# Kernel optimization log

Hardware: AMD Instinct MI355X
Metric: run time of the kernel (lower is better)

## Reference

```python
import jax, jax.numpy as jnp
import numpy as np

T, B, DIM, N = 2048, 16, 1024, 64
INIT_BETA_BIAS = 2.0
EPS = 1e-6


def setup_inputs() -> dict:
    key = jax.random.key(0)
    ks = jax.random.split(key, 6)
    xavier = np.sqrt(2.0 / (N + DIM)).astype(np.float32)
    return {
        "x": jax.random.normal(ks[0], (T, B, DIM), dtype=jnp.float32),
        "S0": jnp.zeros((B, N, N), dtype=jnp.float32),
        "W_k": jax.random.normal(ks[1], (N, DIM), dtype=jnp.float32) * xavier,
        "W_v": jax.random.normal(ks[2], (N, DIM), dtype=jnp.float32) * xavier,
        "W_q": jax.random.normal(ks[3], (N, DIM), dtype=jnp.float32) * xavier,
        "W_beta": jax.random.normal(ks[4], (N, DIM), dtype=jnp.float32) * xavier,
        "b_beta": jnp.full((N,), INIT_BETA_BIAS, dtype=jnp.float32),
    }


def reference(x, S0, W_k, W_v, W_q, W_beta, b_beta):
    # Batched projections: [T, B, dim] @ [dim, n] -> [T, B, n]
    k_all = jnp.einsum("tbd,nd->tbn", x, W_k)
    v_all = jnp.einsum("tbd,nd->tbn", x, W_v)
    q_all = jnp.einsum("tbd,nd->tbn", x, W_q)
    g_all = jax.nn.sigmoid(jnp.einsum("tbd,nd->tbn", x, W_beta) + b_beta)

    def step(S, inp):
        k, v, q, g = inp  # each [B, n]
        k_norm = k / (jnp.linalg.norm(k, axis=-1, keepdims=True) + EPS)
        retrieved = jnp.einsum("bij,bj->bi", S, k_norm)
        delta = v - retrieved
        S_new = g[:, :, None] * S + delta[:, :, None] * k_norm[:, None, :]
        Sq = jnp.einsum("bij,bj->bi", S_new, q)
        out = Sq * jax.nn.silu(Sq)  # self-gated output
        return S_new, out

    S_final, output = jax.lax.scan(step, S0, (k_all, v_all, q_all, g_all))
    return output, S_final
```

## Files before the change

kernel.cpp:

```cpp
#include <hip/hip_runtime.h>
#include <math.h>

#define T_STEPS 2048
#define BATCH   16
#define DIM     1024
#define NSTATE  64
#define NFIELD  256
#define PROJ_TSTRIDE (BATCH * NFIELD)
static constexpr float EPS = 1e-6f;

#define AS1 __attribute__((address_space(1)))
#define AS3 __attribute__((address_space(3)))

typedef _Float16 f16x8 __attribute__((ext_vector_type(8)));
typedef _Float16 f16x4 __attribute__((ext_vector_type(4)));
typedef float    f32x4 __attribute__((ext_vector_type(4)));

template <int CTRL>
__device__ __forceinline__ float dpp_add(float x) {
    int yi = __builtin_amdgcn_update_dpp(0, __float_as_int(x), CTRL, 0xF, 0xF, true);
    return x + __int_as_float(yi);
}
__device__ __forceinline__ float reduce16(float x) {
    x = dpp_add<0x121>(x);
    x = dpp_add<0x122>(x);
    x = dpp_add<0x124>(x);
    x = dpp_add<0x128>(x);
    return x;
}
__device__ __forceinline__ float dot4r(const float4& u, const float4& w) {
    float t0 = u.x * w.x; t0 = fmaf(u.y, w.y, t0);
    float t1 = u.z * w.z; t1 = fmaf(u.w, w.w, t1);
    return reduce16(t0 + t1);
}


#define PBM   128
#define KSTEP 64
#define NKS   (DIM / KSTEP)

__global__ __launch_bounds__(256) void prep_w16(
    const float* __restrict__ Wk, const float* __restrict__ Wv,
    const float* __restrict__ Wq, const float* __restrict__ Wb,
    _Float16* __restrict__ W16)
{
    const int flat = blockIdx.x * 256 + threadIdx.x;
    const int lane = flat & 63;
    const int st   = (flat >> 6) & 31;
    const int ks   = flat >> 11;
    const int cg = st & 15, kc2 = st >> 4;
    const int col = cg * 16 + (lane & 15);
    const int field = col >> 6, wrow = col & 63;
    const float* Wf = (field == 0 ? Wk : field == 1 ? Wv : field == 2 ? Wq : Wb);
    const float* src = Wf + (size_t)wrow * DIM + ks * 64 + kc2 * 32 + (lane >> 4) * 8;
    const float4 a = *(const float4*)(src);
    const float4 b = *(const float4*)(src + 4);
    f16x8 r;
    r[0] = (_Float16)a.x; r[1] = (_Float16)a.y; r[2] = (_Float16)a.z; r[3] = (_Float16)a.w;
    r[4] = (_Float16)b.x; r[5] = (_Float16)b.y; r[6] = (_Float16)b.z; r[7] = (_Float16)b.w;
    *(f16x8*)(W16 + (size_t)flat * 8) = r;
}

__global__ __launch_bounds__(512, 2) void proj_mfma(
    const float* __restrict__ x, const _Float16* __restrict__ W16,
    const float* __restrict__ bb, float* __restrict__ proj)
{
    __shared__ _Float16 Asub[2][16][64][8];
    __shared__ _Float16 Bsub[2][32][64][8];

    const int tid = threadIdx.x;
    const int w = tid >> 6, wl = tid & 63;
    const int wm = w >> 2, wn = w & 3;
    const int l15 = wl & 15, lr = wl >> 4;
    const size_t mbase = (size_t)blockIdx.x * PBM;

    _Float16* const abase = &Asub[0][0][0][0];
    _Float16* const bbase = &Bsub[0][0][0][0];

    const float* asrc[4];
    int aoff[4];
    #pragma unroll
    for (int it = 0; it < 4; ++it) {
        const int fid = it * 512 + tid;
        const int row = fid >> 4, kq = (fid & 15) * 4;
        asrc[it] = x + (mbase + row) * (size_t)DIM + kq;
        aoff[it] = ((kq >> 5) * 8 + (row >> 4)) * 512
                 + ((row & 15) + ((kq >> 3) & 3) * 16) * 8
                 + (kq & 7);
    }
    const _Float16* bsrc[4];
    int boff[4];
    #pragma unroll
    for (int m = 0; m < 4; ++m) {
        const int st = w * 4 + m;
        bsrc[m] = W16 + ((size_t)st * 64 + wl) * 8;
        boff[m] = st * 512;
    }

    auto stageB = [&](int ks, int buf) {
        #pragma unroll
        for (int m = 0; m < 4; ++m) {
            const _Float16* g = bsrc[m] + (size_t)ks * 16384;
            void* lp = (char*)bbase + (size_t)(buf * 16384 + boff[m]) * 2;
            __builtin_amdgcn_global_load_lds((const AS1 void*)g, (AS3 void*)lp, 16, 0, 0);
        }
    };

    float4 ha[4];
    auto loadA = [&](int ks) {
        #pragma unroll
        for (int it = 0; it < 4; ++it)
            ha[it] = *(const float4*)(asrc[it] + ks * KSTEP);
    };
    auto writeA = [&](int buf) {
        #pragma unroll
        for (int it = 0; it < 4; ++it) {
            f16x4 h;
            h[0] = (_Float16)ha[it].x; h[1] = (_Float16)ha[it].y;
            h[2] = (_Float16)ha[it].z; h[3] = (_Float16)ha[it].w;
            *(f16x4*)(abase + buf * 8192 + aoff[it]) = h;
        }
    };

    f32x4 acc[4][4] = {};

    stageB(0, 0);
    loadA(0); writeA(0);
    __syncthreads();

    for (int ks = 0; ks < NKS; ++ks) {
        const int buf = ks & 1;
        if (ks + 1 < NKS) {
            stageB(ks + 1, buf ^ 1);
            loadA(ks + 1);
        }

        #pragma unroll
        for (int kc = 0; kc < 2; ++kc) {
            f16x8 af[4], bf[4];
            #pragma unroll
            for (int mf = 0; mf < 4; ++mf)
                af[mf] = *(const f16x8*)&Asub[buf][kc * 8 + wm * 4 + mf][wl][0];
            #pragma unroll
            for (int nf = 0; nf < 4; ++nf)
                bf[nf] = *(const f16x8*)&Bsub[buf][kc * 16 + wn * 4 + nf][wl][0];
            #pragma unroll
            for (int mf = 0; mf < 4; ++mf)
                #pragma unroll
                for (int nf = 0; nf < 4; ++nf)
                    acc[mf][nf] = __builtin_amdgcn_mfma_f32_16x16x32_f16(
                        af[mf], bf[nf], acc[mf][nf], 0, 0, 0);
        }

        if (ks + 1 < NKS) writeA(buf ^ 1);
        __syncthreads();
    }

    if (wn == 0) {
        #pragma unroll
        for (int mf = 0; mf < 4; ++mf) {
            f32x4 s = acc[mf][0] * acc[mf][0];
            #pragma unroll
            for (int nf = 1; nf < 4; ++nf) s += acc[mf][nf] * acc[mf][nf];
            #pragma unroll
            for (int r = 0; r < 4; ++r) {
                float t = s[r];
                t += __shfl_xor(t, 1); t += __shfl_xor(t, 2);
                t += __shfl_xor(t, 4); t += __shfl_xor(t, 8);
                const float sc = 1.f / (sqrtf(t) + EPS);
                #pragma unroll
                for (int nf = 0; nf < 4; ++nf) acc[mf][nf][r] *= sc;
            }
        }
    }
    if (wn == 3) {
        #pragma unroll
        for (int nf = 0; nf < 4; ++nf) {
            const float bv = bb[nf * 16 + l15];
            #pragma unroll
            for (int mf = 0; mf < 4; ++mf)
                #pragma unroll
                for (int r = 0; r < 4; ++r)
                    acc[mf][nf][r] = 1.f / (1.f + __expf(-(acc[mf][nf][r] + bv)));
        }
    }

    #pragma unroll
    for (int mf = 0; mf < 4; ++mf)
        #pragma unroll
        for (int r = 0; r < 4; ++r) {
            float* dst = proj + (mbase + wm * 64 + mf * 16 + lr * 4 + r) * NFIELD
                              + wn * 64 + l15;
            dst[0]  = acc[mf][0][r];
            dst[16] = acc[mf][1][r];
            dst[32] = acc[mf][2][r];
            dst[48] = acc[mf][3][r];
        }
}

#define KAP_T 2112

__global__ __launch_bounds__(256) void kappa_kernel(
    const float* __restrict__ proj, float* __restrict__ kap)
{
    const int tid = threadIdx.x;
    const int gid = blockIdx.x * 16 + (tid >> 4);
    const int l   = tid & 15;
    const int t = gid >> 4, b = gid & 15;
    if (t == 0 || t >= T_STEPS) {
        if (l == 0) kap[gid] = 0.f;
        return;
    }
    const float4 u = *(const float4*)(proj + ((size_t)t * BATCH + b) * NFIELD + 4 * l);
    const float4 w = *(const float4*)(proj + ((size_t)(t - 1) * BATCH + b) * NFIELD + 4 * l);
    const float p = dot4r(u, w);
    if (l == 0) kap[gid] = p;
}


#define CH 32
#define NCHUNK (T_STEPS / CH)

__global__ __launch_bounds__(128) void scan_kernel(
    const float* __restrict__ proj,
    const float* __restrict__ kap,
    const float* __restrict__ S0,
    float* __restrict__ out,
    float* __restrict__ Sfin)
{
    __shared__ float KQ[2][CH][128];
    __shared__ float VG[2][CH][16];
    __shared__ float KP[2][64];

    const int tid = threadIdx.x;
    const int l   = tid & 15;
    const int grp = tid >> 4;
    const int b   = blockIdx.x >> 3;
    const int i0  = (blockIdx.x & 7) * 8;
    const int i   = i0 + grp;
    const int c0  = l * 4;

    const size_t srow = ((size_t)(b * 64 + i)) * 64 + c0;
    float4 S = *(const float4*)(S0 + srow);

    const float* pb = proj + (size_t)b * NFIELD;
    const int wid = tid >> 6, wl = tid & 63;

    const int l31  = wl & 31;
    const int kq_f = l31 * 4 + ((l31 >= 16) ? 64 : 0);
    const int kq_s = wl >> 5;
    const int idx  = wl & 15;
    const int vg_f = (idx & 1) ? (192 + i0 + (idx >> 1)) : (64 + i0 + (idx >> 1));
    const int vg_s = wl >> 4;

    auto stage = [&](int c, int nb) {
        const float* cbase = pb + (size_t)c * CH * PROJ_TSTRIDE;
        #pragma unroll
        for (int m = 0; m < 8; ++m) {
            const int n = wid * 8 + m;
            const float* g = cbase + (size_t)(2 * n + kq_s) * PROJ_TSTRIDE + kq_f;
            void* lp = (char*)&KQ[nb][0][0] + n * 1024;
            __builtin_amdgcn_global_load_lds((const AS1 void*)g, (AS3 void*)lp, 16, 0, 0);
        }
        #pragma unroll
        for (int m = 0; m < 4; ++m) {
            const int p = wid * 4 + m;
            const float* g = cbase + (size_t)(4 * p + vg_s) * PROJ_TSTRIDE + vg_f;
            void* lp = (char*)&VG[nb][0][0] + p * 256;
            __builtin_amdgcn_global_load_lds((const AS1 void*)g, (AS3 void*)lp, 4, 0, 0);
        }
        if (wid == 0) {
            const float* g = kap + ((size_t)(c * CH + wl + 1) * BATCH + b);
            void* lp = (char*)&KP[nb][0];
            __builtin_amdgcn_global_load_lds((const AS1 void*)g, (AS3 void*)lp, 4, 0, 0);
        }
    };

    float4 kn_s[4], q_s[4];
    float2 vg_s4[4];
    auto ldslot = [&](int cb, int s, int j) {
        kn_s[j]  = *(const float4*)(&KQ[cb][s][c0]);
        q_s[j]   = *(const float4*)(&KQ[cb][s][64 + c0]);
        vg_s4[j] = *(const float2*)(&VG[cb][s][2 * grp]);
    };

    stage(0, 0);
    __syncthreads();

    float a;
    auto prime = [&](int nb) {
        #pragma unroll
        for (int j = 0; j < 4; ++j) ldslot(nb, j, j);
        a = dot4r(S, kn_s[0]);
    };
    prime(0);

    float osel = 0.f;

    for (int c = 0; c < NCHUNK; ++c) {
        const int cb = c & 1;
        const bool more = (c + 1 < NCHUNK);
        if (more) stage(c + 1, cb ^ 1);

        #pragma unroll
        for (int s = 0; s < CH; ++s) {
            const int j = s & 3;
            const float4 kn = kn_s[j], q = q_s[j];
            const float  v = vg_s4[j].x, g = vg_s4[j].y;

            float cpart = 0.f, kap_n = 0.f;
            if (s + 1 < CH) {
                const float4 knn = kn_s[(s + 1) & 3];
                kap_n = KP[cb][s];
                cpart = dot4r(S, knn);
            }

            if (s + 4 < CH) ldslot(cb, s + 4, j);

            const float d = v - a;
            S.x = fmaf(d, kn.x, g * S.x);
            S.y = fmaf(d, kn.y, g * S.y);
            S.z = fmaf(d, kn.z, g * S.z);
            S.w = fmaf(d, kn.w, g * S.w);

            const float sq = dot4r(S, q);
            if (s + 1 < CH) a = fmaf(d, kap_n, g * cpart);

            osel = ((s & 15) == l) ? sq : osel;
            if ((s & 15) == 15) {
                const float y = osel * osel / (1.f + __expf(-osel));
                const int tbase = c * CH + (s - 15);
                out[((size_t)(tbase + l) * BATCH + b) * 64 + i] = y;
            }
        }

        if (more) {
            __syncthreads();
            prime(cb ^ 1);
        }
    }

    *(float4*)(Sfin + srow) = S;
}

extern "C" void kernel_launch(void* const* d_in, const int* in_sizes, int n_in,
                              void* d_out, int out_size, void* d_ws, size_t ws_size,
                              hipStream_t stream) {
    const float* x  = (const float*)d_in[0];
    const float* S0 = (const float*)d_in[1];
    const float* Wk = (const float*)d_in[2];
    const float* Wv = (const float*)d_in[3];
    const float* Wq = (const float*)d_in[4];
    const float* Wb = (const float*)d_in[5];
    const float* bb = (const float*)d_in[6];

    float* out  = (float*)d_out;
    float* Sfin = out + (size_t)T_STEPS * BATCH * NSTATE;

    float*    proj = (float*)d_ws;
    float*    kap  = proj + (size_t)T_STEPS * BATCH * NFIELD;
    _Float16* W16  = (_Float16*)(kap + (size_t)KAP_T * BATCH);

    prep_w16<<<128, 256, 0, stream>>>(Wk, Wv, Wq, Wb, W16);
    proj_mfma<<<(T_STEPS * BATCH) / PBM, 512, 0, stream>>>(x, W16, bb, proj);
    kappa_kernel<<<KAP_T, 256, 0, stream>>>(proj, kap);
    scan_kernel<<<(BATCH * NSTATE) / 8, 128, 0, stream>>>(proj, kap, S0, out, Sfin);
}
```

Baseline: 424.8 us.

## Precompute k·q dot products to shorten scan critical path; deepen A prefetch

The scan previously recomputed S·q after each state update, which put a 16-lane reduction on the serial dependency chain. It now uses S_new·q = g*(S·q) + d*(k·q) with k·q precomputed in the kappa kernel, so both reductions run on the old state and are interleaved. The kappa kernel is reorganised to emit (k_t·k_{t+1}, k_t·q_t) pairs, and the scan's LDS staging is changed to match. The projection GEMM also gains a second register buffer to prefetch A two steps ahead, drops the occupancy hint and fully unrolls the K loop, at the cost of more register pressure.

```diff
diff --git a/kernel.cpp b/kernel.cpp
--- a/kernel.cpp
+++ b/kernel.cpp
@@ -27,6 +27,12 @@
     x = dpp_add<0x124>(x);
     x = dpp_add<0x128>(x);
     return x;
+}
+__device__ __forceinline__ void reduce16x2(float& x, float& y) {
+    x = dpp_add<0x121>(x); y = dpp_add<0x121>(y);
+    x = dpp_add<0x122>(x); y = dpp_add<0x122>(y);
+    x = dpp_add<0x124>(x); y = dpp_add<0x124>(y);
+    x = dpp_add<0x128>(x); y = dpp_add<0x128>(y);
 }
 __device__ __forceinline__ float dot4r(const float4& u, const float4& w) {
     float t0 = u.x * w.x; t0 = fmaf(u.y, w.y, t0);
@@ -61,7 +67,7 @@
     *(f16x8*)(W16 + (size_t)flat * 8) = r;
 }
 
-__global__ __launch_bounds__(512, 2) void proj_mfma(
+__global__ __launch_bounds__(512) void proj_mfma(
     const float* __restrict__ x, const _Float16* __restrict__ W16,
     const float* __restrict__ bb, float* __restrict__ proj)
 {
@@ -106,34 +112,35 @@
         }
     };
 
-    float4 ha[4];
-    auto loadA = [&](int ks) {
+    float4 h0[4], h1[4];
+    auto loadA = [&](int ks, float4* h) {
         #pragma unroll
         for (int it = 0; it < 4; ++it)
-            ha[it] = *(const float4*)(asrc[it] + ks * KSTEP);
-    };
-    auto writeA = [&](int buf) {
+            h[it] = *(const float4*)(asrc[it] + ks * KSTEP);
+    };
+    auto writeA = [&](const float4* h, int buf) {
         #pragma unroll
         for (int it = 0; it < 4; ++it) {
-            f16x4 h;
-            h[0] = (_Float16)ha[it].x; h[1] = (_Float16)ha[it].y;
-            h[2] = (_Float16)ha[it].z; h[3] = (_Float16)ha[it].w;
-            *(f16x4*)(abase + buf * 8192 + aoff[it]) = h;
+            f16x4 v;
+            v[0] = (_Float16)h[it].x; v[1] = (_Float16)h[it].y;
+            v[2] = (_Float16)h[it].z; v[3] = (_Float16)h[it].w;
+            *(f16x4*)(abase + buf * 8192 + aoff[it]) = v;
         }
     };
 
     f32x4 acc[4][4] = {};
 
+    loadA(0, h0);
     stageB(0, 0);
-    loadA(0); writeA(0);
+    loadA(1, h1);
+    writeA(h0, 0);
     __syncthreads();
 
+    #pragma unroll
     for (int ks = 0; ks < NKS; ++ks) {
         const int buf = ks & 1;
-        if (ks + 1 < NKS) {
-            stageB(ks + 1, buf ^ 1);
-            loadA(ks + 1);
-        }
+        if (ks + 1 < NKS) stageB(ks + 1, buf ^ 1);
+        if (ks + 2 < NKS) loadA(ks + 2, (ks & 1) ? h1 : h0);
 
         #pragma unroll
         for (int kc = 0; kc < 2; ++kc) {
@@ -152,7 +159,7 @@
                         af[mf], bf[nf], acc[mf][nf], 0, 0, 0);
         }
 
-        if (ks + 1 < NKS) writeA(buf ^ 1);
+        if (ks + 1 < NKS) writeA((ks & 1) ? h0 : h1, buf ^ 1);
         __syncthreads();
     }
 
@@ -201,20 +208,34 @@
 #define KAP_T 2112
 
 __global__ __launch_bounds__(256) void kappa_kernel(
-    const float* __restrict__ proj, float* __restrict__ kap)
+    const float* __restrict__ proj, float* __restrict__ kap2)
 {
     const int tid = threadIdx.x;
     const int gid = blockIdx.x * 16 + (tid >> 4);
     const int l   = tid & 15;
     const int t = gid >> 4, b = gid & 15;
-    if (t == 0 || t >= T_STEPS) {
-        if (l == 0) kap[gid] = 0.f;
+    if (t >= T_STEPS) {
+        if (l == 0) *(float2*)(kap2 + (size_t)gid * 2) = make_float2(0.f, 0.f);
         return;
     }
-    const float4 u = *(const float4*)(proj + ((size_t)t * BATCH + b) * NFIELD + 4 * l);
-    const float4 w = *(const float4*)(proj + ((size_t)(t - 1) * BATCH + b) * NFIELD + 4 * l);
-    const float p = dot4r(u, w);
-    if (l == 0) kap[gid] = p;
+    const float* base = proj + ((size_t)t * BATCH + b) * NFIELD;
+    const float4 k0 = *(const float4*)(base + 4 * l);
+    const float4 q0 = *(const float4*)(base + 128 + 4 * l);
+    float cp = 0.f;
+    float cq = 0.f;
+    {
+        float t0 = k0.x * q0.x; t0 = fmaf(k0.y, q0.y, t0);
+        float t1 = k0.z * q0.z; t1 = fmaf(k0.w, q0.w, t1);
+        cq = t0 + t1;
+    }
+    if (t + 1 < T_STEPS) {
+        const float4 k1 = *(const float4*)(base + PROJ_TSTRIDE + 4 * l);
+        float t0 = k0.x * k1.x; t0 = fmaf(k0.y, k1.y, t0);
+        float t1 = k0.z * k1.z; t1 = fmaf(k0.w, k1.w, t1);
+        cp = t0 + t1;
+    }
+    reduce16x2(cp, cq);
+    if (l == 0) *(float2*)(kap2 + (size_t)gid * 2) = make_float2(cp, cq);
 }
 
 
@@ -223,14 +244,14 @@
 
 __global__ __launch_bounds__(128) void scan_kernel(
     const float* __restrict__ proj,
-    const float* __restrict__ kap,
+    const float* __restrict__ kap2,
     const float* __restrict__ S0,
     float* __restrict__ out,
     float* __restrict__ Sfin)
 {
     __shared__ float KQ[2][CH][128];
     __shared__ float VG[2][CH][16];
-    __shared__ float KP[2][64];
+    __shared__ float KP2[2][CH][2];
 
     const int tid = threadIdx.x;
     const int l   = tid & 15;
@@ -270,8 +291,9 @@
             __builtin_amdgcn_global_load_lds((const AS1 void*)g, (AS3 void*)lp, 4, 0, 0);
         }
         if (wid == 0) {
-            const float* g = kap + ((size_t)(c * CH + wl + 1) * BATCH + b);
-            void* lp = (char*)&KP[nb][0];
+            const float* g = kap2 + ((size_t)(c * CH + (wl >> 1)) * BATCH + b) * 2
+                           + (wl & 1);
+            void* lp = (char*)&KP2[nb][0][0];
             __builtin_amdgcn_global_load_lds((const AS1 void*)g, (AS3 void*)lp, 4, 0, 0);
         }
     };
@@ -305,17 +327,27 @@
         #pragma unroll
         for (int s = 0; s < CH; ++s) {
             const int j = s & 3;
+
             const float4 kn = kn_s[j], q = q_s[j];
             const float  v = vg_s4[j].x, g = vg_s4[j].y;
-
-            float cpart = 0.f, kap_n = 0.f;
+            const float4 knn = kn_s[(s + 1) & 3];
+            const float2 kk = *(const float2*)&KP2[cb][s][0];
+
+            if (s + 4 < CH) ldslot(cb, s + 4, j);
+
+            float cq;
+            {
+                float t0 = S.x * q.x; t0 = fmaf(S.y, q.y, t0);
+                float t1 = S.z * q.z; t1 = fmaf(S.w, q.w, t1);
+                cq = t0 + t1;
+            }
+            float cp = 0.f;
             if (s + 1 < CH) {
-                const float4 knn = kn_s[(s + 1) & 3];
-                kap_n = KP[cb][s];
-                cpart = dot4r(S, knn);
+                float t0 = S.x * knn.x; t0 = fmaf(S.y, knn.y, t0);
+                float t1 = S.z * knn.z; t1 = fmaf(S.w, knn.w, t1);
+                cp = t0 + t1;
             }
-
-            if (s + 4 < CH) ldslot(cb, s + 4, j);
+            reduce16x2(cp, cq);
 
             const float d = v - a;
             S.x = fmaf(d, kn.x, g * S.x);
@@ -323,8 +355,8 @@
             S.z = fmaf(d, kn.z, g * S.z);
             S.w = fmaf(d, kn.w, g * S.w);
 
-            const float sq = dot4r(S, q);
-            if (s + 1 < CH) a = fmaf(d, kap_n, g * cpart);
+            const float sq = fmaf(d, kk.y, g * cq);
+            if (s + 1 < CH) a = fmaf(d, kk.x, g * cp);
 
             osel = ((s & 15) == l) ? sq : osel;
             if ((s & 15) == 15) {
@@ -358,11 +390,11 @@
     float* Sfin = out + (size_t)T_STEPS * BATCH * NSTATE;
 
     float*    proj = (float*)d_ws;
-    float*    kap  = proj + (size_t)T_STEPS * BATCH * NFIELD;
-    _Float16* W16  = (_Float16*)(kap + (size_t)KAP_T * BATCH);
+    float*    kap2 = proj + (size_t)T_STEPS * BATCH * NFIELD;
+    _Float16* W16  = (_Float16*)(kap2 + (size_t)KAP_T * BATCH * 2);
 
     prep_w16<<<128, 256, 0, stream>>>(Wk, Wv, Wq, Wb, W16);
     proj_mfma<<<(T_STEPS * BATCH) / PBM, 512, 0, stream>>>(x, W16, bb, proj);
-    kappa_kernel<<<KAP_T, 256, 0, stream>>>(proj, kap);
-    scan_kernel<<<(BATCH * NSTATE) / 8, 128, 0, stream>>>(proj, kap, S0, out, Sfin);
-}
+    kappa_kernel<<<KAP_T, 256, 0, stream>>>(proj, kap2);
+    scan_kernel<<<(BATCH * NSTATE) / 8, 128, 0, stream>>>(proj, kap2, S0, out, Sfin);
+}
```

Result: no change. 422.6 us (-0.5%).
